# Kernel optimization log

Measured on AMD Instinct MI355X. Metric: run time of the kernel, lower is better.

## Reference

```python
import jax, jax.numpy as jnp
import numpy as np

# Model hyperparameters (from init_kwargs)
B, N, D = 64, 196, 768      # batch, patches, patch_dim
TKN = 768                   # token dim
QK = 64                     # per-head qk dim
H = 12                      # heads
HN = int(4.0 * TKN)         # Hopfield hidden = 3072
BETA = 1.0 / np.sqrt(QK)    # attn_beta default: 1/sqrt(qk_dim)
BLOCKS = 2
K_STEPS = 4                 # time_steps per block
EPS = 1e-5
ALPHA_RAW0 = float(np.log(np.exp(1.0) - 1.0))  # softplus^-1(alpha_init=1.0)


def setup_inputs() -> dict:
    key = jax.random.key(0)
    ks = jax.random.split(key, 8)
    sd = 0.02
    return {
        "x": jax.random.normal(ks[0], (B, N, D), dtype=jnp.float32),
        "W_enc": jax.random.normal(ks[1], (D, TKN), dtype=jnp.float32) * sd,
        "b_enc": jnp.zeros((TKN,), jnp.float32),
        "cls": jnp.ones((1, 1, TKN), jnp.float32),
        "pos": jax.random.normal(ks[2], (1, N + 1, TKN), dtype=jnp.float32) * sd,
        "gamma": jnp.ones((BLOCKS,), jnp.float32),             # EnergyLayerNorm scalar gain per block
        "bias": jnp.zeros((BLOCKS, TKN), jnp.float32),          # EnergyLayerNorm bias per block
        "Wq": jax.random.normal(ks[3], (BLOCKS, H, QK, TKN), dtype=jnp.float32) * sd,
        "Wk": jax.random.normal(ks[4], (BLOCKS, H, QK, TKN), dtype=jnp.float32) * sd,
        "Whn": jax.random.normal(ks[5], (BLOCKS, TKN, HN), dtype=jnp.float32) * sd,
        "alpha_raw": jnp.full((BLOCKS,), ALPHA_RAW0, jnp.float32),
        "ln_g": jnp.ones((TKN,), jnp.float32),
        "ln_b": jnp.zeros((TKN,), jnp.float32),
        "W_dec": jax.random.normal(ks[6], (TKN, D), dtype=jnp.float32) * sd,
        "b_dec": jnp.zeros((D,), jnp.float32),
    }


def _enorm(x, g_scale, g_bias):
    # EnergyLayerNorm: scalar gamma, per-dim bias, RMS of centered x
    xm = x - x.mean(-1, keepdims=True)
    return g_scale * xm * jax.lax.rsqrt((xm * xm).mean(-1, keepdims=True) + EPS) + g_bias


def _energy(g, Wq, Wk, Whn):
    # Hopfield-attention energy: -1/beta * sum logsumexp(beta * K^T Q)
    q = jnp.einsum("bnd,hzd->bnhz", g, Wq)
    k = jnp.einsum("bnd,hzd->bnhz", g, Wk)
    logits = jnp.einsum("bqhz,bkhz->bhqk", q, k)  # [B,H,N+1,N+1]
    e_attn = -(1.0 / BETA) * jnp.sum(jax.nn.logsumexp(BETA * logits, axis=-1))
    # Hopfield memory energy: -0.5 * sum relu(g W)^2
    e_hn = -0.5 * jnp.sum(jax.nn.relu(g @ Whn) ** 2)
    return e_attn + e_hn


_egrad = jax.grad(_energy)


def reference(x, W_enc, b_enc, cls, pos, gamma, bias, Wq, Wk, Whn, alpha_raw,
              ln_g, ln_b, W_dec, b_dec):
    t = x @ W_enc + b_enc                                   # encode -> [B,N,TKN]
    t = jnp.concatenate([jnp.broadcast_to(cls, (t.shape[0], 1, TKN)), t], axis=1)
    t = t + pos                                             # [B,N+1,TKN]
    for b in range(BLOCKS):
        a = jax.nn.softplus(alpha_raw[b])
        for _ in range(K_STEPS):
            g = _enorm(t, gamma[b], bias[b])
            t = t - a * _egrad(g, Wq[b], Wk[b], Whn[b])
    # decode: standard LayerNorm then Linear
    mu = t.mean(-1, keepdims=True)
    var = ((t - mu) ** 2).mean(-1, keepdims=True)
    h = (t - mu) * jax.lax.rsqrt(var + EPS) * ln_g + ln_b
    out = h @ W_dec + b_dec
    return out[:, 1:]                                       # drop CLS -> [B,N,D]
```

## Files before the change

kernel.cpp:

```cpp
#include <hip/hip_runtime.h>
#include <cstdint>
#include <cstddef>

using u16 = unsigned short;
typedef short short8 __attribute__((ext_vector_type(8)));
typedef short short4v __attribute__((ext_vector_type(4)));
typedef float f32x4 __attribute__((ext_vector_type(4)));

#define LN_EPS 1e-5f
#define ATT_BETA 0.125f

__device__ __forceinline__ u16 f2bf(float f){
  uint32_t u = __float_as_uint(f);
  u += 0x7fffu + ((u >> 16) & 1u);
  return (u16)(u >> 16);
}
__device__ __forceinline__ float bf2f(u16 h){
  return __uint_as_float(((uint32_t)h) << 16);
}
__device__ __forceinline__ float wred_sum(float v){
  #pragma unroll
  for(int o=32;o;o>>=1) v += __shfl_xor(v,o,64);
  return v;
}
__device__ __forceinline__ void async16(const void* g, void* l){
  __builtin_amdgcn_global_load_lds((const __attribute__((address_space(1))) void*)g,
                                   (__attribute__((address_space(3))) void*)l, 16, 0, 0);
}

template<int EPI, int ASPL>
__global__ __launch_bounds__(256)
void gemm_bt(const u16* __restrict__ A, const u16* __restrict__ A2,
             const u16* __restrict__ B,
             u16* __restrict__ Cb, float* __restrict__ Cf,
             int M, int N, int K, int ldb, int ldc,
             const float* __restrict__ aux0, const float* __restrict__ aux1,
             const float* __restrict__ araw, int blk)
{
  __shared__ u16 lA[128*32];
  __shared__ u16 lB[128*32];
  int tid = threadIdx.x;
  int w = tid >> 6, l = tid & 63;
  int wm = w >> 1, wn = w & 1;
  unsigned nwg = gridDim.x*gridDim.y;
  unsigned lin = blockIdx.y*gridDim.x + blockIdx.x;
  unsigned qq = nwg>>3, rr = nwg&7, xcd = lin&7, idx = lin>>3;
  unsigned swz = (xcd<rr ? xcd*(qq+1) : rr*(qq+1) + (xcd-rr)*qq) + idx;
  int m0 = (int)(swz / gridDim.x) * 128, n0 = (int)(swz % gridDim.x) * 128;
  int lr = l >> 2;
  int lc = (l & 3) * 8;
  f32x4 acc[4][4];
  #pragma unroll
  for(int i=0;i<4;i++)
    #pragma unroll
    for(int j=0;j<4;j++) acc[i][j] = (f32x4){0.f,0.f,0.f,0.f};
  int fm = l & 15, fq = (l >> 4) * 8;

  for(int kt=0; kt<K; kt+=32){
    __syncthreads();
    const u16* Asrc = A; int kcol = kt;
    if(ASPL){ if(kt >= 768){ Asrc = A2; kcol = kt - 768; } }
    int lda = ASPL ? 768 : K;
    #pragma unroll
    for(int c=0;c<2;c++){
      int rr2 = (w*2+c)*16;
      int ga = m0 + rr2 + lr; if(ga > M-1) ga = M-1;
      async16(Asrc + (size_t)ga*lda + kcol + lc, &lA[rr2*32]);
      int gb = n0 + rr2 + lr; if(gb > N-1) gb = N-1;
      async16(B + (size_t)gb*ldb + kt + lc, &lB[rr2*32]);
    }
    __syncthreads();
    short8 af[4], bfv[4];
    #pragma unroll
    for(int i=0;i<4;i++) af[i]  = *(const short8*)&lA[(wm*64 + i*16 + fm)*32 + fq];
    #pragma unroll
    for(int j=0;j<4;j++) bfv[j] = *(const short8*)&lB[(wn*64 + j*16 + fm)*32 + fq];
    #pragma unroll
    for(int i=0;i<4;i++)
      #pragma unroll
      for(int j=0;j<4;j++)
        acc[i][j] = __builtin_amdgcn_mfma_f32_16x16x32_bf16(af[i], bfv[j], acc[i][j], 0, 0, 0);
  }

  float alpha = 0.f;
  if(EPI==2) alpha = log1pf(__expf(araw[blk]));

  #pragma unroll
  for(int i=0;i<4;i++){
    int row_b = m0 + wm*64 + i*16 + (l>>4)*4;
    #pragma unroll
    for(int j=0;j<4;j++){
      int col = n0 + wn*64 + j*16 + (l&15);
      #pragma unroll
      for(int r=0;r<4;r++){
        int row = row_b + r;
        if(row >= M) continue;
        float v = acc[i][j][r];
        if(EPI==1){
          Cb[(size_t)row*ldc + col] = f2bf(v > 0.f ? v : 0.f);
        } else if(EPI==2){
          Cf[(size_t)row*768 + col] += alpha * v;
        } else if(EPI==3){
          int pb = row / 196, pn = row - pb*196;
          Cf[((size_t)pb*197 + 1 + pn)*768 + col] = v + aux0[col] + aux1[(size_t)(1+pn)*768 + col];
        } else {
          int pb = row / 197, rr3 = row - pb*197;
          if(rr3 > 0) Cf[((size_t)pb*196 + rr3 - 1)*768 + col] = v + aux0[col];
        }
      }
    }
  }
}

__global__ __launch_bounds__(256)
void norm_k(const float* __restrict__ t, u16* __restrict__ out,
            const float* __restrict__ gv, const float* __restrict__ bv, int blk, int mode)
{
  __shared__ float r1[4], r2[4];
  int row = blockIdx.x;
  const float* tr = t + (size_t)row*768;
  int tid = threadIdx.x, w = tid>>6, l = tid&63;
  f32x4 v = (f32x4){0.f,0.f,0.f,0.f};
  float s=0.f, s2=0.f;
  if(tid < 192){
    v = ((const f32x4*)tr)[tid];
    s  = v[0]+v[1]+v[2]+v[3];
    s2 = v[0]*v[0]+v[1]*v[1]+v[2]*v[2]+v[3]*v[3];
  }
  s = wred_sum(s); s2 = wred_sum(s2);
  if(l==0){ r1[w]=s; r2[w]=s2; }
  __syncthreads();
  s  = r1[0]+r1[1]+r1[2]+r1[3];
  s2 = r2[0]+r2[1]+r2[2]+r2[3];
  float mu  = s * (1.0f/768.0f);
  float var = s2 * (1.0f/768.0f) - mu*mu;
  float rs  = rsqrtf(var + LN_EPS);
  u16* orow = out + (size_t)row*768;
  if(tid < 192){
    short4v o;
    if(mode==0){
      float gm = gv[blk];
      const float* bb = bv + blk*768;
      #pragma unroll
      for(int c=0;c<4;c++) o[c] = (short)f2bf((v[c]-mu)*rs*gm + bb[tid*4+c]);
    } else {
      #pragma unroll
      for(int c=0;c<4;c++) o[c] = (short)f2bf((v[c]-mu)*rs*gv[tid*4+c] + bv[tid*4+c]);
    }
    ((short4v*)orow)[tid] = o;
  }
}

__global__ __launch_bounds__(512, 2)
void attn_fused(const u16* __restrict__ g, const u16* __restrict__ Wqk,
                u16* __restrict__ GqO, u16* __restrict__ GkO)
{
  __shared__ u16 smem[76800];
  __shared__ float SredS[2][4][16];
  u16* Qlds = smem;
  u16* Klds = smem + 14976;
  u16* QTl  = smem + 29952;
  u16* KTl  = smem + 44800;
  u16* P    = smem + 59648;
  u16* PT   = smem + 67840;
  u16* lg   = smem + 59648;

  int bhw = blockIdx.x;
  int bh = (bhw & 7)*96 + (bhw >> 3);
  int b = bh/12, h = bh - b*12;
  const u16* grows = g + (size_t)b*197*768;
  u16* Qg = GqO + (size_t)b*197*768 + h*64;
  u16* Kg = GkO + (size_t)b*197*768 + h*64;
  int tid = threadIdx.x, w = tid>>6, l = tid&63;
  int lane16 = l & 15, quad = l >> 4;

  for(int idx=tid; idx<64*24; idx+=512){
    int z = idx/24, c = 208 + (idx - (idx/24)*24);
    QTl[z*232 + c] = 0; KTl[z*232 + c] = 0;
  }

  {
    int half = w >> 2;
    int wsub = w & 3;
    int rt0 = (wsub==0) ? 0 : 1 + 3*wsub;
    int rtn = (wsub==0) ? 4 : 3;
    const u16* Wb = Wqk + (size_t)half*589824 + (size_t)(h*64)*768;
    u16* Lr = half ? Klds : Qlds;
    u16* Lt = half ? KTl  : QTl;
    f32x4 acc[4][4];
    #pragma unroll
    for(int i=0;i<4;i++)
      #pragma unroll
      for(int z=0;z<4;z++) acc[i][z] = (f32x4){0.f,0.f,0.f,0.f};

    #define STAGE_G(bufi, ktv) do{                                                    \
      { int rw = tid>>2, c4 = tid&3; int r2 = rw>196?196:rw;                          \
        async16(grows + (size_t)r2*768 + (ktv)*32 + c4*8, lg + (bufi)*6656 + tid*8);} \
      int i1 = tid + 512;                                                             \
      if(i1 < 832){ int rw = i1>>2, c4 = i1&3; int r2 = rw>196?196:rw;                \
        async16(grows + (size_t)r2*768 + (ktv)*32 + c4*8, lg + (bufi)*6656 + i1*8);}  \
    }while(0)

    short8 bq[4], bqn[4];
    #pragma unroll
    for(int z=0;z<4;z++) bq[z] = *(const short8*)(Wb + (size_t)(z*16+lane16)*768 + quad*8);
    STAGE_G(0, 0);
    int buf = 0;
    for(int kt=0; kt<24; kt++){
      __syncthreads();
      if(kt < 23){
        STAGE_G(buf^1, kt+1);
        #pragma unroll
        for(int z=0;z<4;z++)
          bqn[z] = *(const short8*)(Wb + (size_t)(z*16+lane16)*768 + (kt+1)*32 + quad*8);
      }
      const u16* lb = lg + buf*6656;
      #pragma unroll
      for(int i=0;i<4;i++) if(i<rtn){
        short8 af = *(const short8*)(lb + (size_t)((rt0+i)*16 + lane16)*32 + quad*8);
        #pragma unroll
        for(int z=0;z<4;z++)
          acc[i][z] = __builtin_amdgcn_mfma_f32_16x16x32_bf16(af, bq[z], acc[i][z],0,0,0);
      }
      #pragma unroll
      for(int z=0;z<4;z++) bq[z] = bqn[z];
      buf ^= 1;
    }
    #undef STAGE_G

    #pragma unroll
    for(int i=0;i<4;i++) if(i<rtn)
      #pragma unroll
      for(int z=0;z<4;z++)
        #pragma unroll
        for(int r=0;r<4;r++){
          int q  = (rt0+i)*16 + quad*4 + r;
          int zz = z*16 + lane16;
          u16 hv = f2bf(acc[i][z][r]);
          Lr[q*72   + zz] = hv;
          Lt[zz*232 + q ] = hv;
        }
  }
  __syncthreads();

  {
    int q = tid>>4, j = 208 + (tid&15);
    P[q*256 + 8*((j>>3)^(q&7)) + (j&7)] = 0;
  }

  int mt = w & 1, nh = w >> 1;
  int ncnt = (nh==0) ? 4 : 3;
  int nt0s = (nh==0) ? 0 : (1 + 3*nh);
  int jt0 = (w<5) ? 2*w : 10+(w-5);
  int jn  = (w<5) ? 2 : 1;

  f32x4 gk[2][4];
  #pragma unroll
  for(int a=0;a<2;a++)
    #pragma unroll
    for(int n2=0;n2<4;n2++) gk[a][n2] = (f32x4){0.f,0.f,0.f,0.f};

  for(int st=0; st<7; st++){
    int q0 = st*32;
    int qa = q0 + 16*mt + lane16; if(qa > 196) qa = 196;
    short8 a0 = *(const short8*)&Qlds[qa*72 + quad*8];
    short8 a1 = *(const short8*)&Qlds[qa*72 + 32 + quad*8];
    f32x4 sa[4];
    #pragma unroll
    for(int ni=0;ni<4;ni++) sa[ni] = (f32x4){0.f,0.f,0.f,0.f};
    for(int ni=0; ni<ncnt; ni++){
      int jb = (nt0s+ni)*16 + lane16; if(jb > 196) jb = 196;
      short8 b0 = *(const short8*)&Klds[jb*72 + quad*8];
      short8 b1 = *(const short8*)&Klds[jb*72 + 32 + quad*8];
      sa[ni] = __builtin_amdgcn_mfma_f32_16x16x32_bf16(a0, b0, sa[ni],0,0,0);
      sa[ni] = __builtin_amdgcn_mfma_f32_16x16x32_bf16(a1, b1, sa[ni],0,0,0);
    }
    for(int ni=0; ni<ncnt; ni++){
      if((nt0s+ni)*16 + lane16 > 196){
        sa[ni][0]=-3e38f; sa[ni][1]=-3e38f; sa[ni][2]=-3e38f; sa[ni][3]=-3e38f;
      }
    }
    float ss[4] = {0.f,0.f,0.f,0.f};
    for(int ni=0; ni<ncnt; ni++)
      #pragma unroll
      for(int r=0;r<4;r++){
        float e = __expf(fminf(ATT_BETA*sa[ni][r], 80.f));
        sa[ni][r] = e; ss[r] += e;
      }
    #pragma unroll
    for(int o=1;o<16;o<<=1)
      #pragma unroll
      for(int r=0;r<4;r++) ss[r] += __shfl_xor(ss[r], o, 64);
    if(lane16==0){
      #pragma unroll
      for(int r=0;r<4;r++) SredS[mt][nh][quad*4+r] = ss[r];
    }
    __syncthreads();
    float inv[4];
    #pragma unroll
    for(int r=0;r<4;r++)
      inv[r] = 1.f/(SredS[mt][0][quad*4+r] + SredS[mt][1][quad*4+r]
                  + SredS[mt][2][quad*4+r] + SredS[mt][3][quad*4+r]);
    for(int ni=0; ni<ncnt; ni++){
      int j = (nt0s+ni)*16 + lane16;
      short4v pk;
      #pragma unroll
      for(int r=0;r<4;r++){
        int q = 16*mt + quad*4 + r;
        float val = (q0 + q <= 196) ? sa[ni][r]*inv[r] : 0.f;
        u16 hv = f2bf(val);
        P[q*256 + 8*((j>>3)^(q&7)) + (j&7)] = hv;
        pk[r] = (short)hv;
      }
      *(short4v*)&PT[j*40 + 16*mt + 4*quad] = pk;
    }
    __syncthreads();
    {
      f32x4 gq = (f32x4){0.f,0.f,0.f,0.f};
      int qrow = 16*mt + lane16;
      int z = nh*16 + lane16;
      for(int kt=0; kt<7; kt++){
        short8 af = *(const short8*)&P[qrow*256 + 8*((4*kt+quad)^(qrow&7))];
        short8 bf8 = *(const short8*)&KTl[z*232 + kt*32 + quad*8];
        gq = __builtin_amdgcn_mfma_f32_16x16x32_bf16(af, bf8, gq,0,0,0);
      }
      #pragma unroll
      for(int r=0;r<4;r++){
        int qg2 = q0 + 16*mt + quad*4 + r;
        if(qg2 <= 196) Qg[(size_t)qg2*768 + nh*16 + lane16] = f2bf(gq[r]);
      }
    }
    {
      short8 bq2[4];
      #pragma unroll
      for(int n2=0;n2<4;n2++)
        bq2[n2] = *(const short8*)&QTl[(n2*16+lane16)*232 + q0 + quad*8];
      for(int ji=0; ji<jn; ji++){
        int j = (jt0+ji)*16 + lane16;
        short8 af = *(const short8*)&PT[j*40 + quad*8];
        #pragma unroll
        for(int n2=0;n2<4;n2++)
          gk[ji][n2] = __builtin_amdgcn_mfma_f32_16x16x32_bf16(af, bq2[n2], gk[ji][n2],0,0,0);
      }
    }
  }
  __syncthreads();
  for(int ji=0; ji<jn; ji++){
    int jt = jt0 + ji;
    #pragma unroll
    for(int n2=0;n2<4;n2++)
      #pragma unroll
      for(int r=0;r<4;r++){
        int j = jt*16 + quad*4 + r;
        if(j <= 196) Kg[(size_t)j*768 + n2*16 + lane16] = f2bf(gk[ji][n2][r]);
      }
  }
}

__global__ void cvt_k(const float* __restrict__ in, u16* __restrict__ out, int n){
  for(int i=blockIdx.x*256+threadIdx.x; i<n; i+=gridDim.x*256) out[i] = f2bf(in[i]);
}

__global__ __launch_bounds__(256)
void tr_k(const float* __restrict__ src, u16* __restrict__ dst, int R, int C, int dstride, int coff){
  __shared__ float tile[32][33];
  int c0 = blockIdx.x*32, r0 = blockIdx.y*32;
  int tx = threadIdx.x & 31, ty = threadIdx.x >> 5;
  for(int i=ty;i<32;i+=8) tile[i][tx] = src[(size_t)(r0+i)*C + c0 + tx];
  __syncthreads();
  for(int i=ty;i<32;i+=8) dst[(size_t)(c0+i)*dstride + coff + r0 + tx] = f2bf(tile[tx][i]);
}

__global__ void fill_cls_k(float* __restrict__ t, const float* __restrict__ cls, const float* __restrict__ pos){
  int b = blockIdx.x;
  for(int i=threadIdx.x;i<768;i+=256) t[(size_t)b*197*768 + i] = cls[i] + pos[i];
}

extern "C" void kernel_launch(void* const* d_in, const int* in_sizes, int n_in,
                              void* d_out, int out_size, void* d_ws, size_t ws_size,
                              hipStream_t stream){
  const float* x      = (const float*)d_in[0];
  const float* W_enc  = (const float*)d_in[1];
  const float* b_enc  = (const float*)d_in[2];
  const float* cls    = (const float*)d_in[3];
  const float* pos    = (const float*)d_in[4];
  const float* gamma  = (const float*)d_in[5];
  const float* bias   = (const float*)d_in[6];
  const float* Wq     = (const float*)d_in[7];
  const float* Wk     = (const float*)d_in[8];
  const float* Whn    = (const float*)d_in[9];
  const float* araw   = (const float*)d_in[10];
  const float* ln_g   = (const float*)d_in[11];
  const float* ln_b   = (const float*)d_in[12];
  const float* W_dec  = (const float*)d_in[13];
  const float* b_dec  = (const float*)d_in[14];
  float* out = (float*)d_out;
  (void)in_sizes; (void)n_in; (void)out_size;

  const int M  = 64*197;
  const int MX = 64*196;

  char* p = (char*)d_ws;
  float* t   = (float*)p;  p += (size_t)M*768*4;
  u16*   g   = (u16*)p;    p += (size_t)M*768*2;
  u16*   Qb  = (u16*)p;    p += (size_t)M*768*2;
  u16*   Kb  = (u16*)p;    p += (size_t)M*768*2;
  size_t base = (size_t)(p - (char*)d_ws);
  if(base > ws_size) return;
  u16* hidden; int hop_merged;
  if(base + (size_t)M*3072*2 <= ws_size){ hidden = (u16*)(d_ws) + base/2; hop_merged = 1; }
  else { hidden = Qb; hop_merged = 0; }

  u16* Wall = (u16*)d_out;
  u16* Wqkb = Wall;
  u16* WqkT = Wall + 2359296;
  u16* WhnT = Wall + 4718592;
  u16* WhnB = Wall + 9437184;
  u16* xb    = Qb;
  u16* WencT = Kb;
  u16* WdecT = Kb;

  for(int b=0;b<2;b++){
    cvt_k<<<512,256,0,stream>>>(Wq + (size_t)b*589824, Wqkb + (size_t)b*1179648, 589824);
    cvt_k<<<512,256,0,stream>>>(Wk + (size_t)b*589824, Wqkb + (size_t)b*1179648 + 589824, 589824);
    tr_k<<<dim3(24,24),256,0,stream>>>(Wq + (size_t)b*589824, WqkT + (size_t)b*1179648, 768,768, 1536, 0);
    tr_k<<<dim3(24,24),256,0,stream>>>(Wk + (size_t)b*589824, WqkT + (size_t)b*1179648, 768,768, 1536, 768);
    tr_k<<<dim3(96,24),256,0,stream>>>(Whn + (size_t)b*2359296, WhnT + (size_t)b*2359296, 768,3072, 768, 0);
    cvt_k<<<2048,256,0,stream>>>(Whn + (size_t)b*2359296, WhnB + (size_t)b*2359296, 2359296);
  }

  cvt_k<<<1024,256,0,stream>>>(x, xb, MX*768);
  tr_k<<<dim3(24,24),256,0,stream>>>(W_enc, WencT, 768,768, 768, 0);
  fill_cls_k<<<64,256,0,stream>>>(t, cls, pos);
  gemm_bt<3,0><<<dim3(6,98),256,0,stream>>>(xb, nullptr, WencT, nullptr, t,
                                            MX, 768, 768, 768, 768,
                                            b_enc, pos, nullptr, 0);

  for(int blk=0; blk<2; blk++){
    for(int s=0; s<4; s++){
      norm_k<<<M,256,0,stream>>>(t, g, gamma, bias, blk, 0);
      if(hop_merged){
        gemm_bt<1,0><<<dim3(24,99),256,0,stream>>>(g, nullptr,
            WhnT + (size_t)blk*2359296,
            hidden, nullptr, M, 3072, 768, 768, 3072,
            nullptr, nullptr, nullptr, 0);
        gemm_bt<2,0><<<dim3(6,99),256,0,stream>>>(hidden, nullptr,
            WhnB + (size_t)blk*2359296,
            nullptr, t, M, 768, 3072, 3072, 768,
            nullptr, nullptr, araw, blk);
      } else {
        for(int c=0;c<2;c++){
          gemm_bt<1,0><<<dim3(12,99),256,0,stream>>>(g, nullptr,
              WhnT + (size_t)blk*2359296 + (size_t)c*1536*768,
              hidden, nullptr, M, 1536, 768, 768, 1536,
              nullptr, nullptr, nullptr, 0);
          gemm_bt<2,0><<<dim3(6,99),256,0,stream>>>(hidden, nullptr,
              WhnB + (size_t)blk*2359296 + (size_t)c*1536,
              nullptr, t, M, 768, 1536, 3072, 768,
              nullptr, nullptr, araw, blk);
        }
      }
      attn_fused<<<768,512,0,stream>>>(g, Wqkb + (size_t)blk*1179648, Qb, Kb);
      gemm_bt<2,1><<<dim3(6,99),256,0,stream>>>(Qb, Kb, WqkT + (size_t)blk*1179648,
            nullptr, t, M, 768, 1536, 1536, 768,
            nullptr, nullptr, araw, blk);
    }
  }

  tr_k<<<dim3(24,24),256,0,stream>>>(W_dec, WdecT, 768,768, 768, 0);
  norm_k<<<M,256,0,stream>>>(t, g, ln_g, ln_b, 0, 1);
  gemm_bt<4,0><<<dim3(6,99),256,0,stream>>>(g, nullptr, WdecT, nullptr, out,
                                            M, 768, 768, 768, 768,
                                            b_dec, nullptr, nullptr, 0);
}
```

Baseline: 4.031 ms.

## Double-buffer GEMM LDS tiles and move P zero-padding into the attention loop

The GEMM main loop now uses two LDS buffers per operand. It issues the async global-to-LDS loads for the next K-slice before computing the current one, so each iteration needs only one barrier and load latency overlaps the MFMAs. In the attention kernel, the zeroing of the padded P columns moves inside the per-step loop, and a barrier is added at the start of each step to guard buffer reuse. This doubles GEMM shared-memory use, which may lower occupancy, and adds barriers to the attention kernel.

New measurement: 3.809 ms. -5.5%, faster.

```diff
diff --git a/kernel.cpp b/kernel.cpp
--- a/kernel.cpp
+++ b/kernel.cpp
@@ -37,8 +37,8 @@
              const float* __restrict__ aux0, const float* __restrict__ aux1,
              const float* __restrict__ araw, int blk)
 {
-  __shared__ u16 lA[128*32];
-  __shared__ u16 lB[128*32];
+  __shared__ u16 lA[2][128*32];
+  __shared__ u16 lB[2][128*32];
   int tid = threadIdx.x;
   int w = tid >> 6, l = tid & 63;
   int wm = w >> 1, wn = w & 1;
@@ -56,31 +56,39 @@
     for(int j=0;j<4;j++) acc[i][j] = (f32x4){0.f,0.f,0.f,0.f};
   int fm = l & 15, fq = (l >> 4) * 8;
 
+  #define STAGE_AB(bufi, ktv) do{                                            \
+    const u16* Asrc = A; int kcol = (ktv);                                   \
+    if(ASPL){ if((ktv) >= 768){ Asrc = A2; kcol = (ktv) - 768; } }           \
+    int lda = ASPL ? 768 : K;                                                \
+    _Pragma("unroll")                                                        \
+    for(int c=0;c<2;c++){                                                    \
+      int rr2 = (w*2+c)*16;                                                  \
+      int ga = m0 + rr2 + lr; if(ga > M-1) ga = M-1;                         \
+      async16(Asrc + (size_t)ga*lda + kcol + lc, &lA[bufi][rr2*32]);         \
+      int gb = n0 + rr2 + lr; if(gb > N-1) gb = N-1;                         \
+      async16(B + (size_t)gb*ldb + (ktv) + lc, &lB[bufi][rr2*32]);           \
+    }                                                                        \
+  }while(0)
+
+  STAGE_AB(0, 0);
+  __syncthreads();
+  int buf = 0;
   for(int kt=0; kt<K; kt+=32){
-    __syncthreads();
-    const u16* Asrc = A; int kcol = kt;
-    if(ASPL){ if(kt >= 768){ Asrc = A2; kcol = kt - 768; } }
-    int lda = ASPL ? 768 : K;
-    #pragma unroll
-    for(int c=0;c<2;c++){
-      int rr2 = (w*2+c)*16;
-      int ga = m0 + rr2 + lr; if(ga > M-1) ga = M-1;
-      async16(Asrc + (size_t)ga*lda + kcol + lc, &lA[rr2*32]);
-      int gb = n0 + rr2 + lr; if(gb > N-1) gb = N-1;
-      async16(B + (size_t)gb*ldb + kt + lc, &lB[rr2*32]);
-    }
-    __syncthreads();
+    if(kt+32 < K) STAGE_AB(buf^1, kt+32);
     short8 af[4], bfv[4];
     #pragma unroll
-    for(int i=0;i<4;i++) af[i]  = *(const short8*)&lA[(wm*64 + i*16 + fm)*32 + fq];
-    #pragma unroll
-    for(int j=0;j<4;j++) bfv[j] = *(const short8*)&lB[(wn*64 + j*16 + fm)*32 + fq];
+    for(int i=0;i<4;i++) af[i]  = *(const short8*)&lA[buf][(wm*64 + i*16 + fm)*32 + fq];
+    #pragma unroll
+    for(int j=0;j<4;j++) bfv[j] = *(const short8*)&lB[buf][(wn*64 + j*16 + fm)*32 + fq];
     #pragma unroll
     for(int i=0;i<4;i++)
       #pragma unroll
       for(int j=0;j<4;j++)
         acc[i][j] = __builtin_amdgcn_mfma_f32_16x16x32_bf16(af[i], bfv[j], acc[i][j], 0, 0, 0);
-  }
+    __syncthreads();
+    buf ^= 1;
+  }
+  #undef STAGE_AB
 
   float alpha = 0.f;
   if(EPI==2) alpha = log1pf(__expf(araw[blk]));
@@ -243,11 +251,6 @@
   }
   __syncthreads();
 
-  {
-    int q = tid>>4, j = 208 + (tid&15);
-    P[q*256 + 8*((j>>3)^(q&7)) + (j&7)] = 0;
-  }
-
   int mt = w & 1, nh = w >> 1;
   int ncnt = (nh==0) ? 4 : 3;
   int nt0s = (nh==0) ? 0 : (1 + 3*nh);
@@ -262,6 +265,7 @@
 
   for(int st=0; st<7; st++){
     int q0 = st*32;
+    __syncthreads();
     int qa = q0 + 16*mt + lane16; if(qa > 196) qa = 196;
     short8 a0 = *(const short8*)&Qlds[qa*72 + quad*8];
     short8 a1 = *(const short8*)&Qlds[qa*72 + 32 + quad*8];
@@ -313,6 +317,10 @@
         pk[r] = (short)hv;
       }
       *(short4v*)&PT[j*40 + 16*mt + 4*quad] = pk;
+    }
+    for(int idx=tid; idx<32*16; idx+=512){
+      int q = idx>>4, j = 208 + (idx&15);
+      P[q*256 + 8*((j>>3)^(q&7)) + (j&7)] = 0;
     }
     __syncthreads();
     {
```
